# Performance work log

Measured on AMD Instinct MI355X. Metric: run time of the kernel, lower is better.

## Reference

```python
import jax, jax.numpy as jnp
import numpy as np

N, E = 100000, 1000000          # nodes, edges
IN, OUT = 64, 64                # feature dims
R, B = 16, 8                    # num_rels, num_bases


def setup_inputs() -> dict:
    key = jax.random.key(0)
    k = jax.random.split(key, 6)
    h = jax.random.normal(k[0], (N, IN), jnp.float32)
    weight = jax.random.normal(k[1], (B, IN, OUT), jnp.float32) * 0.05
    w_comp = jax.random.normal(k[2], (R, B), jnp.float32) * 0.3
    src = jax.random.randint(k[3], (E,), 0, N, jnp.int32)
    dst = jax.random.randint(k[4], (E,), 0, N, jnp.int32)
    rel = jax.random.randint(k[5], (E,), 0, R, jnp.int32)
    return {"h": h, "weight": weight, "w_comp": w_comp,
            "src": src, "dst": dst, "rel": rel}


def _rel_weights(weight, w_comp):
    # Faithful replication of the torch basis-combination including its
    # exact (reinterpreting) view calls:
    #   weight.view(in, B, out); matmul(w_comp, .); .view(R, in, out)
    V = weight.reshape(IN, B, OUT)                 # reinterpret, not transpose
    M = jnp.einsum('rb,ibo->iro', w_comp, V)       # [IN, R, OUT]
    return M.reshape(R, IN, OUT)


def reference(h, weight, w_comp, src, dst, rel):
    W = _rel_weights(weight, w_comp)               # [R, IN, OUT]
    # msg_e = h[src_e] @ W[rel_e]; computed without materializing [E,IN,OUT]:
    proj = jnp.einsum('nd,rdf->nrf', h, W)         # [N, R, OUT]
    msg = proj[src, rel]                           # [E, OUT] per-edge gather
    h2 = jax.ops.segment_sum(msg, dst, num_segments=N)  # fn.sum -> 'h2'
    # apply_func: bias is None (falsy); returns activation(old h).
    # Note: original apply_func reads but does not use h2 (tutorial quirk);
    # we return both the updated 'h' and the aggregated 'h2'.
    h_new = jax.nn.relu(h)
    return h_new, h2
```

## Files before the change

### kernel.cpp

```cpp
#include <hip/hip_runtime.h>
#include <hip/hip_bf16.h>

#define NN 100000
#define EE 1000000
#define FDIM 64
#define NREL 16
#define NBASE 8
#define HN (NN * FDIM)
#define H4 (HN / 4)
#define WSZ (NREL * FDIM * FDIM)
#define NPAD 100032
#define PCOLS 1024
#define NB_SCAN ((NN + 255) / 256)
#define EGX 128

typedef __attribute__((ext_vector_type(8))) short short8;
typedef __attribute__((ext_vector_type(4))) float f32x4;

static __device__ __forceinline__ ushort f2bf(float f) {
    __hip_bfloat16 b = __float2bfloat16(f);
    return *(ushort*)&b;
}
static __device__ __forceinline__ float bf2f(ushort u) {
    unsigned x = ((unsigned)u) << 16;
    float f;
    __builtin_memcpy(&f, &x, 4);
    return f;
}

__global__ void prep_kernel(const float4* __restrict__ h4, float4* __restrict__ out4,
                            ushort2* __restrict__ hb2,
                            const float* __restrict__ weight,
                            const float* __restrict__ w_comp, ushort* __restrict__ WT,
                            int* __restrict__ cnt, int czn,
                            float4* __restrict__ h2z, int zero_h2) {
    int gid = blockIdx.x * blockDim.x + threadIdx.x;
    if (gid < czn) cnt[gid] = 0;
    if (gid < WSZ) {
        int r = gid >> 12;
        int o = (gid >> 6) & 63;
        int d = gid & 63;
        const float* wc = w_comp + (d & 15) * NBASE;
        const float* wv = weight + (size_t)(4 * r + (d >> 4)) * 512 + o;
        float acc = 0.f;
#pragma unroll
        for (int b = 0; b < NBASE; ++b)
            acc = fmaf(wc[b], wv[b * 64], acc);
        WT[gid] = f2bf(acc);
    }
    if (gid < H4) {
        float4 v = h4[gid];
        ushort2 lo, hi;
        lo.x = f2bf(v.x); lo.y = f2bf(v.y);
        hi.x = f2bf(v.z); hi.y = f2bf(v.w);
        hb2[2 * gid] = lo;
        hb2[2 * gid + 1] = hi;
        v.x = fmaxf(v.x, 0.f); v.y = fmaxf(v.y, 0.f);
        v.z = fmaxf(v.z, 0.f); v.w = fmaxf(v.w, 0.f);
        out4[gid] = v;
        if (zero_h2) h2z[gid] = make_float4(0.f, 0.f, 0.f, 0.f);
    }
}


__global__ __launch_bounds__(256) void proj_gemm_kernel(
    const ushort* __restrict__ hb, const ushort* __restrict__ WT,
    ushort* __restrict__ projb, const int* __restrict__ dst, int* __restrict__ cnt) {
    const int wv = threadIdx.x >> 6;
    const int lane = threadIdx.x & 63;
    const int quad = lane >> 4, l15 = lane & 15;
    const int row0 = blockIdx.x * 64;
    const int col0 = blockIdx.y * 256 + wv * 64;

    if (blockIdx.y == 0) {
        int tid = blockIdx.x * 256 + threadIdx.x;
        int stride = gridDim.x * 256;
        for (int i = tid; i < EE; i += stride)
            atomicAdd(&cnt[dst[i]], 1);
    }

    short8 Af[4][2];
#pragma unroll
    for (int g = 0; g < 4; ++g) {
        const short8* ar = (const short8*)(hb + (size_t)(row0 + 16 * g + l15) * 64);
        Af[g][0] = ar[quad];
        Af[g][1] = ar[4 + quad];
    }
    short8 Bf[2][4];
#pragma unroll
    for (int t = 0; t < 4; ++t) {
        const short8* br = (const short8*)(WT + (size_t)(col0 + 16 * t + l15) * 64);
        Bf[0][t] = br[quad];
        Bf[1][t] = br[4 + quad];
    }
    f32x4 acc[4][4];
#pragma unroll
    for (int g = 0; g < 4; ++g)
#pragma unroll
        for (int t = 0; t < 4; ++t) acc[g][t] = (f32x4){0.f, 0.f, 0.f, 0.f};
#pragma unroll
    for (int g = 0; g < 4; ++g)
#pragma unroll
        for (int t = 0; t < 4; ++t) {
            acc[g][t] = __builtin_amdgcn_mfma_f32_16x16x32_bf16(Af[g][0], Bf[0][t], acc[g][t], 0, 0, 0);
            acc[g][t] = __builtin_amdgcn_mfma_f32_16x16x32_bf16(Af[g][1], Bf[1][t], acc[g][t], 0, 0, 0);
        }
#pragma unroll
    for (int g = 0; g < 4; ++g) {
        int rbase = row0 + 16 * g + quad * 4;
#pragma unroll
        for (int t = 0; t < 4; ++t) {
            size_t cb = (size_t)(col0 + 16 * t + l15);
#pragma unroll
            for (int r = 0; r < 4; ++r)
                projb[(size_t)(rbase + r) * PCOLS + cb] = f2bf(acc[g][t][r]);
        }
    }
}

__global__ __launch_bounds__(256) void scan_a_kernel(const int* __restrict__ cnt,
                                                     int* __restrict__ bsum) {
    int i = blockIdx.x * 256 + threadIdx.x;
    int v = (i < NN) ? cnt[i] : 0;
#pragma unroll
    for (int o = 32; o > 0; o >>= 1) v += __shfl_down(v, o, 64);
    __shared__ int ws4[4];
    if ((threadIdx.x & 63) == 0) ws4[threadIdx.x >> 6] = v;
    __syncthreads();
    if (threadIdx.x == 0) bsum[blockIdx.x] = ws4[0] + ws4[1] + ws4[2] + ws4[3];
}

__global__ __launch_bounds__(512) void scan_b_kernel(const int* __restrict__ bsum,
                                                     int* __restrict__ bbase,
                                                     int* __restrict__ off) {
    __shared__ int lds[512];
    int t = threadIdx.x;
    int v = (t < NB_SCAN) ? bsum[t] : 0;
    lds[t] = v;
    __syncthreads();
    for (int o = 1; o < 512; o <<= 1) {
        int u = (t >= o) ? lds[t - o] : 0;
        __syncthreads();
        lds[t] += u;
        __syncthreads();
    }
    if (t < NB_SCAN) bbase[t] = lds[t] - v;
    if (t == NB_SCAN - 1) off[NN] = lds[t];
}

__global__ __launch_bounds__(256) void scan_c_kernel(const int* __restrict__ cnt,
                                                     const int* __restrict__ bbase,
                                                     int* __restrict__ off,
                                                     int* __restrict__ cur) {
    __shared__ int lds[256];
    int i = blockIdx.x * 256 + threadIdx.x;
    int t = threadIdx.x;
    int v = (i < NN) ? cnt[i] : 0;
    lds[t] = v;
    __syncthreads();
    for (int o = 1; o < 256; o <<= 1) {
        int u = (t >= o) ? lds[t - o] : 0;
        __syncthreads();
        lds[t] += u;
        __syncthreads();
    }
    if (i < NN) {
        int excl = lds[t] - v + bbase[blockIdx.x];
        off[i] = excl;
        cur[i] = excl;
    }
}

__global__ void scatter_dst_kernel(const int* __restrict__ src, const int* __restrict__ dst,
                                   const int* __restrict__ rel, int* __restrict__ cur,
                                   int* __restrict__ pidx) {
    int i = blockIdx.x * blockDim.x + threadIdx.x;
    if (i < EE) {
        int pos = atomicAdd(&cur[dst[i]], 1);
        pidx[pos] = src[i] * 16 + rel[i];
    }
}

__global__ __launch_bounds__(256) void aggregate_kernel(
    const int* __restrict__ off, const int* __restrict__ pidx,
    const ushort* __restrict__ projb, float* __restrict__ h2) {
    int wv = (blockIdx.x * 256 + threadIdx.x) >> 6;
    int lane = threadIdx.x & 63;
    int v = __builtin_amdgcn_readfirstlane(wv);
    if (v >= NN) return;
    int s = off[v], e = off[v + 1];
    float acc = 0.f;
    int i = s;
    for (; i + 4 <= e; i += 4) {
        int p0 = pidx[i], p1 = pidx[i + 1], p2 = pidx[i + 2], p3 = pidx[i + 3];
        float a = bf2f(projb[(size_t)p0 * 64 + lane]);
        float b = bf2f(projb[(size_t)p1 * 64 + lane]);
        float c = bf2f(projb[(size_t)p2 * 64 + lane]);
        float d = bf2f(projb[(size_t)p3 * 64 + lane]);
        acc += (a + b) + (c + d);
    }
    for (; i < e; ++i)
        acc += bf2f(projb[(size_t)pidx[i] * 64 + lane]);
    h2[(size_t)v * 64 + lane] = acc;
}


__global__ void hist16_kernel(const int* __restrict__ rel, int* __restrict__ counts) {
    __shared__ int lc[NREL];
    if (threadIdx.x < NREL) lc[threadIdx.x] = 0;
    __syncthreads();
    int stride = gridDim.x * blockDim.x;
    for (int i = blockIdx.x * blockDim.x + threadIdx.x; i < EE; i += stride)
        atomicAdd(&lc[rel[i]], 1);
    __syncthreads();
    if (threadIdx.x < NREL && lc[threadIdx.x] > 0)
        atomicAdd(&counts[threadIdx.x], lc[threadIdx.x]);
}

__global__ void scan16_kernel(const int* __restrict__ counts,
                              int* __restrict__ offsets, int* __restrict__ cursors) {
    if (threadIdx.x == 0 && blockIdx.x == 0) {
        int acc = 0;
        for (int r = 0; r < NREL; ++r) { offsets[r] = acc; cursors[r] = acc; acc += counts[r]; }
        offsets[NREL] = acc;
    }
}

__global__ void scatter16_kernel(const int* __restrict__ rel, const int* __restrict__ src,
                                 const int* __restrict__ dst, int* __restrict__ cursors,
                                 int* __restrict__ src_bin, int* __restrict__ dst_bin) {
    __shared__ int lhist[NREL];
    __shared__ int lbase[NREL];
    int i = blockIdx.x * blockDim.x + threadIdx.x;
    if (threadIdx.x < NREL) lhist[threadIdx.x] = 0;
    __syncthreads();
    int r = 0, rank = 0;
    if (i < EE) { r = rel[i]; rank = atomicAdd(&lhist[r], 1); }
    __syncthreads();
    if (threadIdx.x < NREL && lhist[threadIdx.x] > 0)
        lbase[threadIdx.x] = atomicAdd(&cursors[threadIdx.x], lhist[threadIdx.x]);
    __syncthreads();
    if (i < EE) {
        int pos = lbase[r] + rank;
        src_bin[pos] = src[i];
        dst_bin[pos] = dst[i];
    }
}

__global__ __launch_bounds__(256) void edge_mfma_kernel(
    const int* __restrict__ offsets, const int* __restrict__ src_bin,
    const int* __restrict__ dst_bin, const ushort* __restrict__ hb,
    const ushort* __restrict__ WT, float* __restrict__ h2) {
    const int rel = blockIdx.y;
    const int lane = threadIdx.x & 63;
    const int quad = lane >> 4;
    const int l15 = lane & 15;
    const int start = offsets[rel];
    const int end = offsets[rel + 1];
    const int cnt = end - start;
    if (cnt <= 0) return;

    const short8* wt = (const short8*)(WT + rel * 4096);
    short8 Bf[2][4];
#pragma unroll
    for (int t = 0; t < 4; ++t) {
#pragma unroll
        for (int s = 0; s < 2; ++s)
            Bf[s][t] = wt[((t * 16 + l15) << 3) + (s << 2) + quad];
    }
    const int nw = EGX * 4;
    const int wave = blockIdx.x * 4 + (threadIdx.x >> 6);
    const int nb = (cnt + 15) >> 4;
    const int per = (nb + nw - 1) / nw;
    int b0 = wave * per;
    int b1 = b0 + per; if (b1 > nb) b1 = nb;
    const int quad4 = quad * 4;

    for (int b = b0; b < b1; ++b) {
        const int base = start + (b << 4);
        int ei = base + l15; if (ei >= end) ei = end - 1;
        int s0 = src_bin[ei];
        const short8* ar = (const short8*)(hb + (size_t)s0 * FDIM);
        short8 A0 = ar[quad];
        short8 A1 = ar[4 + quad];
        f32x4 acc[4];
#pragma unroll
        for (int t = 0; t < 4; ++t) acc[t] = (f32x4){0.f, 0.f, 0.f, 0.f};
#pragma unroll
        for (int t = 0; t < 4; ++t) {
            acc[t] = __builtin_amdgcn_mfma_f32_16x16x32_bf16(A0, Bf[0][t], acc[t], 0, 0, 0);
            acc[t] = __builtin_amdgcn_mfma_f32_16x16x32_bf16(A1, Bf[1][t], acc[t], 0, 0, 0);
        }
#pragma unroll
        for (int r = 0; r < 4; ++r) {
            int em = base + quad4 + r;
            if (em < end) {
                int dv = dst_bin[em];
                float* p = h2 + (size_t)dv * FDIM + l15;
                unsafeAtomicAdd(p,      acc[0][r]);
                unsafeAtomicAdd(p + 16, acc[1][r]);
                unsafeAtomicAdd(p + 32, acc[2][r]);
                unsafeAtomicAdd(p + 48, acc[3][r]);
            }
        }
    }
}

extern "C" void kernel_launch(void* const* d_in, const int* in_sizes, int n_in,
                              void* d_out, int out_size, void* d_ws, size_t ws_size,
                              hipStream_t stream) {
    const float* h      = (const float*)d_in[0];
    const float* weight = (const float*)d_in[1];
    const float* w_comp = (const float*)d_in[2];
    const int*   src    = (const int*)d_in[3];
    const int*   dst    = (const int*)d_in[4];
    const int*   rel    = (const int*)d_in[5];

    float* out_hnew = (float*)d_out;
    float* out_h2   = out_hnew + HN;

    char* ws = (char*)d_ws;

    size_t o_cnt  = 131072;
    size_t o_off  = o_cnt + 400000;
    size_t o_cur  = o_off + 400016;
    size_t o_pidx = o_cur + 400000;
    size_t o_bsum = o_pidx + 4000000;
    size_t o_bbas = o_bsum + 4 * ((NB_SCAN + 3) & ~3);
    size_t o_hb   = o_bbas + 4 * ((NB_SCAN + 3) & ~3);
    size_t o_proj = o_hb + (size_t)NPAD * 128;
    size_t need   = o_proj + (size_t)NPAD * 2048;

    if (ws_size >= need) {
        ushort* WT    = (ushort*)ws;
        int*    cnt   = (int*)(ws + o_cnt);
        int*    off   = (int*)(ws + o_off);
        int*    cur   = (int*)(ws + o_cur);
        int*    pidx  = (int*)(ws + o_pidx);
        int*    bsum  = (int*)(ws + o_bsum);
        int*    bbase = (int*)(ws + o_bbas);
        ushort* hb    = (ushort*)(ws + o_hb);
        ushort* projb = (ushort*)(ws + o_proj);

        hipLaunchKernelGGL(prep_kernel, dim3((H4 + 255) / 256), dim3(256), 0, stream,
                           (const float4*)h, (float4*)out_hnew, (ushort2*)hb,
                           weight, w_comp, WT, cnt, NN, (float4*)out_h2, 0);
        hipLaunchKernelGGL(proj_gemm_kernel, dim3(NPAD / 64, 4), dim3(256), 0, stream,
                           hb, WT, projb, dst, cnt);
        hipLaunchKernelGGL(scan_a_kernel, dim3(NB_SCAN), dim3(256), 0, stream, cnt, bsum);
        hipLaunchKernelGGL(scan_b_kernel, dim3(1), dim3(512), 0, stream, bsum, bbase, off);
        hipLaunchKernelGGL(scan_c_kernel, dim3(NB_SCAN), dim3(256), 0, stream,
                           cnt, bbase, off, cur);
        hipLaunchKernelGGL(scatter_dst_kernel, dim3((EE + 255) / 256), dim3(256), 0, stream,
                           src, dst, rel, cur, pidx);
        hipLaunchKernelGGL(aggregate_kernel, dim3(NN / 4), dim3(256), 0, stream,
                           off, pidx, projb, out_h2);
    } else {
        ushort* WT      = (ushort*)ws;
        int*    meta    = (int*)(ws + 0x20000);
        int*    counts  = meta;
        int*    offsets = meta + 16;
        int*    cursors = meta + 33;
        int*    src_bin = (int*)(ws + 0x20400);
        int*    dst_bin = (int*)(ws + 0x20400 + 4 * EE);
        ushort* hb      = (ushort*)(ws + 0x20400 + 8 * EE);

        hipLaunchKernelGGL(prep_kernel, dim3((H4 + 255) / 256), dim3(256), 0, stream,
                           (const float4*)h, (float4*)out_hnew, (ushort2*)hb,
                           weight, w_comp, WT, counts, 16, (float4*)out_h2, 1);
        hipLaunchKernelGGL(hist16_kernel, dim3(1024), dim3(256), 0, stream, rel, counts);
        hipLaunchKernelGGL(scan16_kernel, dim3(1), dim3(64), 0, stream,
                           counts, offsets, cursors);
        hipLaunchKernelGGL(scatter16_kernel, dim3((EE + 255) / 256), dim3(256), 0, stream,
                           rel, src, dst, cursors, src_bin, dst_bin);
        hipLaunchKernelGGL(edge_mfma_kernel, dim3(EGX, NREL), dim3(256), 0, stream,
                           offsets, src_bin, dst_bin, hb, WT, out_h2);
    }
}
```

Measured before the change: 338.1 us.

## Reassociate basis combination: aggregate per-relation basis coefficients, then project per node

Replaces the per-node all-relation projection table with a reassociation. A small per-node G = h·w_comp coefficient tensor (32 floats per node) is computed in prep. Edges are then summed into a per-node [rel×32] tile in shared memory, and one MFMA GEMM per 16-node tile against the bf16 basis weights produces h2 directly. The large projection buffer write and read and the fallback relation-binned path are removed. Precision uses a split hi/lo bf16 trick (three MFMAs). The shared-memory accumulation is a non-atomic per-thread add, which relies on each lane owning its own column. Random-access G gathers replace the bf16 proj gathers.

```diff
diff --git a/kernel.cpp b/kernel.cpp
--- a/kernel.cpp
+++ b/kernel.cpp
@@ -8,11 +8,7 @@
 #define NBASE 8
 #define HN (NN * FDIM)
 #define H4 (HN / 4)
-#define WSZ (NREL * FDIM * FDIM)
-#define NPAD 100032
-#define PCOLS 1024
 #define NB_SCAN ((NN + 255) / 256)
-#define EGX 128
 
 typedef __attribute__((ext_vector_type(8))) short short8;
 typedef __attribute__((ext_vector_type(4))) float f32x4;
@@ -28,94 +24,62 @@
     return f;
 }
 
-__global__ void prep_kernel(const float4* __restrict__ h4, float4* __restrict__ out4,
-                            ushort2* __restrict__ hb2,
-                            const float* __restrict__ weight,
-                            const float* __restrict__ w_comp, ushort* __restrict__ WT,
-                            int* __restrict__ cnt, int czn,
-                            float4* __restrict__ h2z, int zero_h2) {
-    int gid = blockIdx.x * blockDim.x + threadIdx.x;
-    if (gid < czn) cnt[gid] = 0;
-    if (gid < WSZ) {
-        int r = gid >> 12;
-        int o = (gid >> 6) & 63;
-        int d = gid & 63;
-        const float* wc = w_comp + (d & 15) * NBASE;
-        const float* wv = weight + (size_t)(4 * r + (d >> 4)) * 512 + o;
-        float acc = 0.f;
-#pragma unroll
-        for (int b = 0; b < NBASE; ++b)
-            acc = fmaf(wc[b], wv[b * 64], acc);
-        WT[gid] = f2bf(acc);
+
+__global__ __launch_bounds__(256) void prep2_kernel(
+    const float4* __restrict__ h4, float4* __restrict__ out4,
+    const float* __restrict__ h, const float* __restrict__ weight,
+    const float* __restrict__ w_comp, float* __restrict__ G,
+    ushort* __restrict__ WbTh, ushort* __restrict__ WbTl,
+    int* __restrict__ cnt) {
+    __shared__ float wc[128];
+    if (threadIdx.x < 128) wc[threadIdx.x] = w_comp[threadIdx.x];
+    __syncthreads();
+    int gid = blockIdx.x * 256 + threadIdx.x;
+    if (gid < NN) cnt[gid] = 0;
+    if (gid < 32768) {
+        int o = gid >> 9, k = gid & 511;
+        float w = weight[k * 64 + o];
+        ushort hi = f2bf(w);
+        WbTh[gid] = hi;
+        WbTl[gid] = f2bf(w - bf2f(hi));
+    }
+    if (gid < NN * 4) {
+        int n = gid >> 2, q = gid & 3;
+        const float4* hp = (const float4*)(h + (size_t)n * 64 + q * 16);
+        float hv[16];
+#pragma unroll
+        for (int m4 = 0; m4 < 4; ++m4) {
+            float4 v = hp[m4];
+            hv[4 * m4 + 0] = v.x; hv[4 * m4 + 1] = v.y;
+            hv[4 * m4 + 2] = v.z; hv[4 * m4 + 3] = v.w;
+        }
+        float accb[8];
+#pragma unroll
+        for (int b = 0; b < 8; ++b) accb[b] = 0.f;
+#pragma unroll
+        for (int m = 0; m < 16; ++m) {
+            float hm = hv[m];
+#pragma unroll
+            for (int b = 0; b < 8; ++b)
+                accb[b] = fmaf(hm, wc[m * 8 + b], accb[b]);
+        }
+        float4* gp = (float4*)(G + (size_t)gid * 8);
+        gp[0] = make_float4(accb[0], accb[1], accb[2], accb[3]);
+        gp[1] = make_float4(accb[4], accb[5], accb[6], accb[7]);
     }
     if (gid < H4) {
         float4 v = h4[gid];
-        ushort2 lo, hi;
-        lo.x = f2bf(v.x); lo.y = f2bf(v.y);
-        hi.x = f2bf(v.z); hi.y = f2bf(v.w);
-        hb2[2 * gid] = lo;
-        hb2[2 * gid + 1] = hi;
         v.x = fmaxf(v.x, 0.f); v.y = fmaxf(v.y, 0.f);
         v.z = fmaxf(v.z, 0.f); v.w = fmaxf(v.w, 0.f);
         out4[gid] = v;
-        if (zero_h2) h2z[gid] = make_float4(0.f, 0.f, 0.f, 0.f);
-    }
-}
-
-
-__global__ __launch_bounds__(256) void proj_gemm_kernel(
-    const ushort* __restrict__ hb, const ushort* __restrict__ WT,
-    ushort* __restrict__ projb, const int* __restrict__ dst, int* __restrict__ cnt) {
-    const int wv = threadIdx.x >> 6;
-    const int lane = threadIdx.x & 63;
-    const int quad = lane >> 4, l15 = lane & 15;
-    const int row0 = blockIdx.x * 64;
-    const int col0 = blockIdx.y * 256 + wv * 64;
-
-    if (blockIdx.y == 0) {
-        int tid = blockIdx.x * 256 + threadIdx.x;
-        int stride = gridDim.x * 256;
-        for (int i = tid; i < EE; i += stride)
-            atomicAdd(&cnt[dst[i]], 1);
-    }
-
-    short8 Af[4][2];
-#pragma unroll
-    for (int g = 0; g < 4; ++g) {
-        const short8* ar = (const short8*)(hb + (size_t)(row0 + 16 * g + l15) * 64);
-        Af[g][0] = ar[quad];
-        Af[g][1] = ar[4 + quad];
-    }
-    short8 Bf[2][4];
-#pragma unroll
-    for (int t = 0; t < 4; ++t) {
-        const short8* br = (const short8*)(WT + (size_t)(col0 + 16 * t + l15) * 64);
-        Bf[0][t] = br[quad];
-        Bf[1][t] = br[4 + quad];
-    }
-    f32x4 acc[4][4];
-#pragma unroll
-    for (int g = 0; g < 4; ++g)
-#pragma unroll
-        for (int t = 0; t < 4; ++t) acc[g][t] = (f32x4){0.f, 0.f, 0.f, 0.f};
-#pragma unroll
-    for (int g = 0; g < 4; ++g)
-#pragma unroll
-        for (int t = 0; t < 4; ++t) {
-            acc[g][t] = __builtin_amdgcn_mfma_f32_16x16x32_bf16(Af[g][0], Bf[0][t], acc[g][t], 0, 0, 0);
-            acc[g][t] = __builtin_amdgcn_mfma_f32_16x16x32_bf16(Af[g][1], Bf[1][t], acc[g][t], 0, 0, 0);
-        }
-#pragma unroll
-    for (int g = 0; g < 4; ++g) {
-        int rbase = row0 + 16 * g + quad * 4;
-#pragma unroll
-        for (int t = 0; t < 4; ++t) {
-            size_t cb = (size_t)(col0 + 16 * t + l15);
-#pragma unroll
-            for (int r = 0; r < 4; ++r)
-                projb[(size_t)(rbase + r) * PCOLS + cb] = f2bf(acc[g][t][r]);
-        }
-    }
+    }
+}
+
+__global__ __launch_bounds__(256) void histn_kernel(const int* __restrict__ dst,
+                                                    int* __restrict__ cnt) {
+    int stride = gridDim.x * 256;
+    for (int i = blockIdx.x * 256 + threadIdx.x; i < EE; i += stride)
+        atomicAdd(&cnt[dst[i]], 1);
 }
 
 __global__ __launch_bounds__(256) void scan_a_kernel(const int* __restrict__ cnt,
@@ -181,129 +145,65 @@
     }
 }
 
-__global__ __launch_bounds__(256) void aggregate_kernel(
+__global__ __launch_bounds__(256) void agg_proj_kernel(
     const int* __restrict__ off, const int* __restrict__ pidx,
-    const ushort* __restrict__ projb, float* __restrict__ h2) {
-    int wv = (blockIdx.x * 256 + threadIdx.x) >> 6;
-    int lane = threadIdx.x & 63;
-    int v = __builtin_amdgcn_readfirstlane(wv);
-    if (v >= NN) return;
-    int s = off[v], e = off[v + 1];
-    float acc = 0.f;
-    int i = s;
-    for (; i + 4 <= e; i += 4) {
-        int p0 = pidx[i], p1 = pidx[i + 1], p2 = pidx[i + 2], p3 = pidx[i + 3];
-        float a = bf2f(projb[(size_t)p0 * 64 + lane]);
-        float b = bf2f(projb[(size_t)p1 * 64 + lane]);
-        float c = bf2f(projb[(size_t)p2 * 64 + lane]);
-        float d = bf2f(projb[(size_t)p3 * 64 + lane]);
-        acc += (a + b) + (c + d);
-    }
-    for (; i < e; ++i)
-        acc += bf2f(projb[(size_t)pidx[i] * 64 + lane]);
-    h2[(size_t)v * 64 + lane] = acc;
-}
-
-
-__global__ void hist16_kernel(const int* __restrict__ rel, int* __restrict__ counts) {
-    __shared__ int lc[NREL];
-    if (threadIdx.x < NREL) lc[threadIdx.x] = 0;
-    __syncthreads();
-    int stride = gridDim.x * blockDim.x;
-    for (int i = blockIdx.x * blockDim.x + threadIdx.x; i < EE; i += stride)
-        atomicAdd(&lc[rel[i]], 1);
-    __syncthreads();
-    if (threadIdx.x < NREL && lc[threadIdx.x] > 0)
-        atomicAdd(&counts[threadIdx.x], lc[threadIdx.x]);
-}
-
-__global__ void scan16_kernel(const int* __restrict__ counts,
-                              int* __restrict__ offsets, int* __restrict__ cursors) {
-    if (threadIdx.x == 0 && blockIdx.x == 0) {
-        int acc = 0;
-        for (int r = 0; r < NREL; ++r) { offsets[r] = acc; cursors[r] = acc; acc += counts[r]; }
-        offsets[NREL] = acc;
-    }
-}
-
-__global__ void scatter16_kernel(const int* __restrict__ rel, const int* __restrict__ src,
-                                 const int* __restrict__ dst, int* __restrict__ cursors,
-                                 int* __restrict__ src_bin, int* __restrict__ dst_bin) {
-    __shared__ int lhist[NREL];
-    __shared__ int lbase[NREL];
-    int i = blockIdx.x * blockDim.x + threadIdx.x;
-    if (threadIdx.x < NREL) lhist[threadIdx.x] = 0;
-    __syncthreads();
-    int r = 0, rank = 0;
-    if (i < EE) { r = rel[i]; rank = atomicAdd(&lhist[r], 1); }
-    __syncthreads();
-    if (threadIdx.x < NREL && lhist[threadIdx.x] > 0)
-        lbase[threadIdx.x] = atomicAdd(&cursors[threadIdx.x], lhist[threadIdx.x]);
-    __syncthreads();
-    if (i < EE) {
-        int pos = lbase[r] + rank;
-        src_bin[pos] = src[i];
-        dst_bin[pos] = dst[i];
-    }
-}
-
-__global__ __launch_bounds__(256) void edge_mfma_kernel(
-    const int* __restrict__ offsets, const int* __restrict__ src_bin,
-    const int* __restrict__ dst_bin, const ushort* __restrict__ hb,
-    const ushort* __restrict__ WT, float* __restrict__ h2) {
-    const int rel = blockIdx.y;
-    const int lane = threadIdx.x & 63;
-    const int quad = lane >> 4;
-    const int l15 = lane & 15;
-    const int start = offsets[rel];
-    const int end = offsets[rel + 1];
-    const int cnt = end - start;
-    if (cnt <= 0) return;
-
-    const short8* wt = (const short8*)(WT + rel * 4096);
-    short8 Bf[2][4];
-#pragma unroll
-    for (int t = 0; t < 4; ++t) {
-#pragma unroll
-        for (int s = 0; s < 2; ++s)
-            Bf[s][t] = wt[((t * 16 + l15) << 3) + (s << 2) + quad];
-    }
-    const int nw = EGX * 4;
-    const int wave = blockIdx.x * 4 + (threadIdx.x >> 6);
-    const int nb = (cnt + 15) >> 4;
-    const int per = (nb + nw - 1) / nw;
-    int b0 = wave * per;
-    int b1 = b0 + per; if (b1 > nb) b1 = nb;
-    const int quad4 = quad * 4;
-
-    for (int b = b0; b < b1; ++b) {
-        const int base = start + (b << 4);
-        int ei = base + l15; if (ei >= end) ei = end - 1;
-        int s0 = src_bin[ei];
-        const short8* ar = (const short8*)(hb + (size_t)s0 * FDIM);
-        short8 A0 = ar[quad];
-        short8 A1 = ar[4 + quad];
-        f32x4 acc[4];
-#pragma unroll
-        for (int t = 0; t < 4; ++t) acc[t] = (f32x4){0.f, 0.f, 0.f, 0.f};
-#pragma unroll
-        for (int t = 0; t < 4; ++t) {
-            acc[t] = __builtin_amdgcn_mfma_f32_16x16x32_bf16(A0, Bf[0][t], acc[t], 0, 0, 0);
-            acc[t] = __builtin_amdgcn_mfma_f32_16x16x32_bf16(A1, Bf[1][t], acc[t], 0, 0, 0);
-        }
-#pragma unroll
-        for (int r = 0; r < 4; ++r) {
-            int em = base + quad4 + r;
-            if (em < end) {
-                int dv = dst_bin[em];
-                float* p = h2 + (size_t)dv * FDIM + l15;
-                unsafeAtomicAdd(p,      acc[0][r]);
-                unsafeAtomicAdd(p + 16, acc[1][r]);
-                unsafeAtomicAdd(p + 32, acc[2][r]);
-                unsafeAtomicAdd(p + 48, acc[3][r]);
+    const float* __restrict__ G, const ushort* __restrict__ WbTh,
+    const ushort* __restrict__ WbTl, float* __restrict__ h2) {
+    __shared__ __align__(16) float T[16][516];
+    int t = threadIdx.x;
+    float* Tf = &T[0][0];
+    for (int i = t; i < 16 * 516; i += 256) Tf[i] = 0.f;
+    __syncthreads();
+
+    const int node0 = blockIdx.x * 16;
+    const int wv = t >> 6;
+    {
+        const int half = (t >> 5) & 1;
+        const int j = t & 31;
+#pragma unroll
+        for (int s = 0; s < 2; ++s) {
+            const int nl = (wv << 2) + (half << 1) + s;
+            int e0 = off[node0 + nl];
+            int e1 = off[node0 + nl + 1];
+            float* trow = &T[nl][0];
+            for (int e = e0; e < e1; ++e) {
+                int p = pidx[e];
+                float g = G[((size_t)(p >> 4) << 5) + j];
+                trow[((p & 15) << 5) + j] += g;
             }
         }
     }
+    __syncthreads();
+
+    const int lane = t & 63;
+    const int quad = lane >> 4, l15 = lane & 15;
+    f32x4 acc0 = (f32x4){0.f, 0.f, 0.f, 0.f};
+    f32x4 acc1 = acc0, acc2 = acc0;
+    const short8* bh = (const short8*)(WbTh + (size_t)(wv * 16 + l15) * 512);
+    const short8* bl = (const short8*)(WbTl + (size_t)(wv * 16 + l15) * 512);
+#pragma unroll
+    for (int kk = 0; kk < 16; ++kk) {
+        const float* ap = &T[l15][kk * 32 + quad * 8];
+        f32x4 a0 = *(const f32x4*)ap;
+        f32x4 a1 = *(const f32x4*)(ap + 4);
+        float av[8] = {a0[0], a0[1], a0[2], a0[3], a1[0], a1[1], a1[2], a1[3]};
+        short8 ah, al;
+#pragma unroll
+        for (int i = 0; i < 8; ++i) {
+            ushort hi = f2bf(av[i]);
+            ah[i] = (short)hi;
+            al[i] = (short)f2bf(av[i] - bf2f(hi));
+        }
+        short8 bhv = bh[kk * 4 + quad];
+        short8 blv = bl[kk * 4 + quad];
+        acc0 = __builtin_amdgcn_mfma_f32_16x16x32_bf16(ah, bhv, acc0, 0, 0, 0);
+        acc1 = __builtin_amdgcn_mfma_f32_16x16x32_bf16(ah, blv, acc1, 0, 0, 0);
+        acc2 = __builtin_amdgcn_mfma_f32_16x16x32_bf16(al, bhv, acc2, 0, 0, 0);
+    }
+    float* hp = h2 + (size_t)(node0 + quad * 4) * 64 + wv * 16 + l15;
+#pragma unroll
+    for (int r = 0; r < 4; ++r)
+        hp[(size_t)r * 64] = acc0[r] + acc1[r] + acc2[r];
 }
 
 extern "C" void kernel_launch(void* const* d_in, const int* in_sizes, int n_in,
@@ -321,59 +221,26 @@
 
     char* ws = (char*)d_ws;
 
-    size_t o_cnt  = 131072;
-    size_t o_off  = o_cnt + 400000;
-    size_t o_cur  = o_off + 400016;
-    size_t o_pidx = o_cur + 400000;
-    size_t o_bsum = o_pidx + 4000000;
-    size_t o_bbas = o_bsum + 4 * ((NB_SCAN + 3) & ~3);
-    size_t o_hb   = o_bbas + 4 * ((NB_SCAN + 3) & ~3);
-    size_t o_proj = o_hb + (size_t)NPAD * 128;
-    size_t need   = o_proj + (size_t)NPAD * 2048;
-
-    if (ws_size >= need) {
-        ushort* WT    = (ushort*)ws;
-        int*    cnt   = (int*)(ws + o_cnt);
-        int*    off   = (int*)(ws + o_off);
-        int*    cur   = (int*)(ws + o_cur);
-        int*    pidx  = (int*)(ws + o_pidx);
-        int*    bsum  = (int*)(ws + o_bsum);
-        int*    bbase = (int*)(ws + o_bbas);
-        ushort* hb    = (ushort*)(ws + o_hb);
-        ushort* projb = (ushort*)(ws + o_proj);
-
-        hipLaunchKernelGGL(prep_kernel, dim3((H4 + 255) / 256), dim3(256), 0, stream,
-                           (const float4*)h, (float4*)out_hnew, (ushort2*)hb,
-                           weight, w_comp, WT, cnt, NN, (float4*)out_h2, 0);
-        hipLaunchKernelGGL(proj_gemm_kernel, dim3(NPAD / 64, 4), dim3(256), 0, stream,
-                           hb, WT, projb, dst, cnt);
-        hipLaunchKernelGGL(scan_a_kernel, dim3(NB_SCAN), dim3(256), 0, stream, cnt, bsum);
-        hipLaunchKernelGGL(scan_b_kernel, dim3(1), dim3(512), 0, stream, bsum, bbase, off);
-        hipLaunchKernelGGL(scan_c_kernel, dim3(NB_SCAN), dim3(256), 0, stream,
-                           cnt, bbase, off, cur);
-        hipLaunchKernelGGL(scatter_dst_kernel, dim3((EE + 255) / 256), dim3(256), 0, stream,
-                           src, dst, rel, cur, pidx);
-        hipLaunchKernelGGL(aggregate_kernel, dim3(NN / 4), dim3(256), 0, stream,
-                           off, pidx, projb, out_h2);
-    } else {
-        ushort* WT      = (ushort*)ws;
-        int*    meta    = (int*)(ws + 0x20000);
-        int*    counts  = meta;
-        int*    offsets = meta + 16;
-        int*    cursors = meta + 33;
-        int*    src_bin = (int*)(ws + 0x20400);
-        int*    dst_bin = (int*)(ws + 0x20400 + 4 * EE);
-        ushort* hb      = (ushort*)(ws + 0x20400 + 8 * EE);
-
-        hipLaunchKernelGGL(prep_kernel, dim3((H4 + 255) / 256), dim3(256), 0, stream,
-                           (const float4*)h, (float4*)out_hnew, (ushort2*)hb,
-                           weight, w_comp, WT, counts, 16, (float4*)out_h2, 1);
-        hipLaunchKernelGGL(hist16_kernel, dim3(1024), dim3(256), 0, stream, rel, counts);
-        hipLaunchKernelGGL(scan16_kernel, dim3(1), dim3(64), 0, stream,
-                           counts, offsets, cursors);
-        hipLaunchKernelGGL(scatter16_kernel, dim3((EE + 255) / 256), dim3(256), 0, stream,
-                           rel, src, dst, cursors, src_bin, dst_bin);
-        hipLaunchKernelGGL(edge_mfma_kernel, dim3(EGX, NREL), dim3(256), 0, stream,
-                           offsets, src_bin, dst_bin, hb, WT, out_h2);
-    }
-}
+    ushort* WbTh  = (ushort*)ws;
+    ushort* WbTl  = (ushort*)(ws + 65536);
+    int*    cnt   = (int*)(ws + 131072);
+    int*    off   = (int*)(ws + 531072);
+    int*    cur   = (int*)(ws + 931088);
+    int*    pidx  = (int*)(ws + 1331088);
+    int*    bsum  = (int*)(ws + 5331088);
+    int*    bbase = (int*)(ws + 5332656);
+    float*  G     = (float*)(ws + 5334224);
+
+    hipLaunchKernelGGL(prep2_kernel, dim3(H4 / 256), dim3(256), 0, stream,
+                       (const float4*)h, (float4*)out_hnew, h, weight, w_comp,
+                       G, WbTh, WbTl, cnt);
+    hipLaunchKernelGGL(histn_kernel, dim3(1024), dim3(256), 0, stream, dst, cnt);
+    hipLaunchKernelGGL(scan_a_kernel, dim3(NB_SCAN), dim3(256), 0, stream, cnt, bsum);
+    hipLaunchKernelGGL(scan_b_kernel, dim3(1), dim3(512), 0, stream, bsum, bbase, off);
+    hipLaunchKernelGGL(scan_c_kernel, dim3(NB_SCAN), dim3(256), 0, stream,
+                       cnt, bbase, off, cur);
+    hipLaunchKernelGGL(scatter_dst_kernel, dim3((EE + 255) / 256), dim3(256), 0, stream,
+                       src, dst, rel, cur, pidx);
+    hipLaunchKernelGGL(agg_proj_kernel, dim3(NN / 16), dim3(256), 0, stream,
+                       off, pidx, G, WbTh, WbTl, out_h2);
+}
```

Result: slower. 386.4 us (+14.3%).
